# Performance work log

Hardware: AMD Instinct MI355X
Metric: run time of the kernel (lower is better)

## Reference

```python
import jax, jax.numpy as jnp
import numpy as np

S, B, IN, H = 512, 128, 256, 512  # seq_len, batch, input_size, hidden_size


def setup_inputs() -> dict:
    key = jax.random.key(0)
    ks = jax.random.split(key, 17)
    def p(k, shape):
        return jax.random.normal(k, shape, dtype=jnp.float32) * 0.05
    inp = {
        "x": jax.random.normal(ks[0], (S, B, IN), dtype=jnp.float32),
        "h0": jnp.zeros((1, B, H), dtype=jnp.float32),
        "c0": jnp.zeros((1, B, H), dtype=jnp.float32),
    }
    # gates: f=forget, i=input, o=output, g=cell candidate
    for j, n in enumerate(["f", "i", "o", "g"]):
        inp[f"W{n}"] = p(ks[1 + 4 * j], (H, IN))
        inp[f"bW{n}"] = p(ks[2 + 4 * j], (H,))
        inp[f"U{n}"] = p(ks[3 + 4 * j], (H, H))
        inp[f"bU{n}"] = p(ks[4 + 4 * j], (H,))
    return inp


def reference(x, h0, c0, Wf, bWf, Uf, bUf, Wi, bWi, Ui, bUi,
              Wo, bWo, Uo, bUo, Wg, bWg, Ug, bUg):
    # Fuse the 4 input projections and 4 recurrent projections into single GEMMs.
    # Math is identical to applying each Linear separately.
    Wcat = jnp.concatenate([Wf, Wi, Wo, Wg], axis=0)      # [4H, IN]
    bcat = jnp.concatenate([bWf + bUf, bWi + bUi, bWo + bUo, bWg + bUg])  # [4H]
    Ucat = jnp.concatenate([Uf, Ui, Uo, Ug], axis=0)      # [4H, H]
    hd = h0.shape[-1]
    # Precompute input-dependent gate pre-activations for all timesteps.
    xg = jnp.einsum('sbi,gi->sbg', x, Wcat) + bcat        # [S, B, 4H]

    def step(carry, xg_t):
        h, c = carry
        g = xg_t + h @ Ucat.T                             # [B, 4H]
        f = jax.nn.sigmoid(g[..., :hd])
        i = jax.nn.sigmoid(g[..., hd:2 * hd])
        o = jax.nn.sigmoid(g[..., 2 * hd:3 * hd])
        cand = jnp.tanh(g[..., 3 * hd:])
        c = f * c + i * cand
        h = o * jnp.tanh(c)
        return (h, c), h

    (h, c), h_seq = jax.lax.scan(step, (h0[-1], c0[-1]), xg)
    return h_seq, h, c
```

## Files before the change

### kernel.cpp

```cpp
#include <hip/hip_runtime.h>
#include <hip/hip_cooperative_groups.h>

namespace cg = cooperative_groups;


#define SQ   512
#define BB   128
#define IN_  256
#define HH   512
#define RG   8
#define CGN  32
#define RINGHALF (BB * HH)
#define RING_OFF 1024

typedef float    f32x4 __attribute__((ext_vector_type(4)));
typedef short    s16x8 __attribute__((ext_vector_type(8)));
typedef unsigned u32x4 __attribute__((ext_vector_type(4)));

struct P {
  const float *x, *h0, *c0;
  const float *W[4], *bW[4], *U[4], *bU[4];
  float* out;
  unsigned* ring;
  int mode;
};

__device__ __forceinline__ unsigned f2b(float f) {
  unsigned u = __float_as_uint(f);
  return (u + 0x7FFFu + ((u >> 16) & 1u)) >> 16;
}
__device__ __forceinline__ float sigm(float x) { return 1.f / (1.f + __expf(-x)); }
__device__ __forceinline__ float tanh_(float x) {
  float e = __expf(-2.f * fabsf(x));
  float t = (1.f - e) / (1.f + e);
  return copysignf(t, x);
}
__device__ __forceinline__ u32x4 pack8(f32x4 a, f32x4 b) {
  u32x4 d;
  d.x = f2b(a.x) | (f2b(a.y) << 16);
  d.y = f2b(a.z) | (f2b(a.w) << 16);
  d.z = f2b(b.x) | (f2b(b.y) << 16);
  d.w = f2b(b.z) | (f2b(b.w) << 16);
  return d;
}

#define LOAD8_LLC(c0_,c1_,c2_,c3_,c4_,c5_,c6_,c7_,ptr_)                      \
  asm volatile(                                                              \
    "global_load_dwordx4 %0, %8, off sc0 sc1\n\t"                            \
    "global_load_dwordx4 %1, %8, off offset:256 sc0 sc1\n\t"                 \
    "global_load_dwordx4 %2, %8, off offset:512 sc0 sc1\n\t"                 \
    "global_load_dwordx4 %3, %8, off offset:768 sc0 sc1\n\t"                 \
    "global_load_dwordx4 %4, %8, off offset:1024 sc0 sc1\n\t"                \
    "global_load_dwordx4 %5, %8, off offset:1280 sc0 sc1\n\t"                \
    "global_load_dwordx4 %6, %8, off offset:1536 sc0 sc1\n\t"                \
    "global_load_dwordx4 %7, %8, off offset:1792 sc0 sc1\n\t"                \
    "s_waitcnt vmcnt(0)"                                                     \
    : "=&v"(c0_), "=&v"(c1_), "=&v"(c2_), "=&v"(c3_),                        \
      "=&v"(c4_), "=&v"(c5_), "=&v"(c6_), "=&v"(c7_)                         \
    : "v"(ptr_) : "memory")

__global__ void __launch_bounds__(256, 1) lstm_all(P p) {
  __shared__ unsigned short Hs[16][512];
  __shared__ unsigned short Xs[2][16][256];
  __shared__ float gbuf[4][16][17];

  const int tid = threadIdx.x;
  const int bid = blockIdx.x;
  const int r   = bid & 7;
  const int cgi = bid >> 3;
  const int rb  = r * 16;
  const int hcb = cgi * 16;

  const int w   = tid >> 6;
  const int l   = tid & 63;
  const int l16 = l & 15;
  const int lk  = l >> 4;
  const int row16 = tid >> 4;
  const int n16   = tid & 15;

  unsigned* ring = p.ring;

  const int col = hcb + l16;
  s16x8 bfrag[24];
#pragma unroll
  for (int kk = 0; kk < 24; ++kk) {
    int k = kk * 32 + lk * 8;
    const float* src = (kk < 8) ? (p.W[w] + (size_t)col * IN_ + k)
                                : (p.U[w] + (size_t)col * HH + (k - IN_));
    f32x4 a = *(const f32x4*)src;
    f32x4 b = *(const f32x4*)(src + 4);
    s16x8 v;
    v[0]=(short)f2b(a.x); v[1]=(short)f2b(a.y); v[2]=(short)f2b(a.z); v[3]=(short)f2b(a.w);
    v[4]=(short)f2b(b.x); v[5]=(short)f2b(b.y); v[6]=(short)f2b(b.z); v[7]=(short)f2b(b.w);
    bfrag[kk] = v;
  }
  const float bias = p.bW[w][col] + p.bU[w][col];
  float cval = p.c0[(size_t)(rb + row16) * HH + hcb + n16];

  const int wswz = (row16 & 7) << 4;
  const int rswz = (l16 & 7) << 4;
  char* HsB = (char*)&Hs[0][0];
  char* XsB = (char*)&Xs[0][0][0];

  f32x4 xg0, xg1, xg2, xg3;
  {
    const float* xs = p.x + (size_t)(rb + row16) * IN_ + n16 * 16;
    xg0 = *(const f32x4*)(xs);
    xg1 = *(const f32x4*)(xs + 4);
    xg2 = *(const f32x4*)(xs + 8);
    xg3 = *(const f32x4*)(xs + 12);
  }

  for (int t = 0; t < SQ; ++t) {
    {
      char* xrow = XsB + (t & 1) * 8192 + row16 * 512;
      *(u32x4*)(xrow + ((n16 * 32)      ^ wswz)) = pack8(xg0, xg1);
      *(u32x4*)(xrow + ((n16 * 32 + 16) ^ wswz)) = pack8(xg2, xg3);
      if (t + 1 < SQ) {
        const float* xs = p.x + ((size_t)(t + 1) * BB + rb + row16) * IN_ + n16 * 16;
        xg0 = *(const f32x4*)(xs);
        xg1 = *(const f32x4*)(xs + 4);
        xg2 = *(const f32x4*)(xs + 8);
        xg3 = *(const f32x4*)(xs + 12);
      }
    }

    char* hrow = HsB + row16 * 1024;
    if (t == 0) {
      const float* src = p.h0 + (size_t)(rb + row16) * HH + n16 * 4;
#pragma unroll
      for (int cc = 0; cc < 8; ++cc) {
        f32x4 v = *(const f32x4*)(src + cc * 64);
        unsigned lo = f2b(v.x) | (f2b(v.y) << 16);
        unsigned hi = f2b(v.z) | (f2b(v.w) << 16);
        int boff = ((cc * 128 + n16 * 8) ^ wswz);
        *(uint2*)(hrow + boff) = make_uint2(lo, hi);
      }
    } else if (p.mode == 0) {
      const unsigned* hb = ring + (((t - 1) & 1) ? RINGHALF : 0)
                         + (size_t)(rb + row16) * HH + n16 * 4;
      u32x4 c0,c1,c2,c3,c4,c5,c6,c7;
      const unsigned tg = (unsigned)t;
#define TAGOK(v) (((v).x >> 16) == tg && ((v).y >> 16) == tg && \
                  ((v).z >> 16) == tg && ((v).w >> 16) == tg)
      int spin = 0;
      for (;;) {
        LOAD8_LLC(c0,c1,c2,c3,c4,c5,c6,c7,hb);
        if (TAGOK(c0) && TAGOK(c1) && TAGOK(c2) && TAGOK(c3) &&
            TAGOK(c4) && TAGOK(c5) && TAGOK(c6) && TAGOK(c7)) break;
        if (++spin > (1 << 16)) break;
        if (spin > 8) __builtin_amdgcn_s_sleep(1);
      }
#undef TAGOK
      u32x4 cv[8] = {c0,c1,c2,c3,c4,c5,c6,c7};
#pragma unroll
      for (int cc = 0; cc < 8; ++cc) {
        unsigned lo = (cv[cc].x & 0xFFFFu) | (cv[cc].y << 16);
        unsigned hi = (cv[cc].z & 0xFFFFu) | (cv[cc].w << 16);
        int boff = ((cc * 128 + n16 * 8) ^ wswz);
        *(uint2*)(hrow + boff) = make_uint2(lo, hi);
      }
    } else {
      cg::this_grid().sync();
      const float* hp = p.out + ((size_t)(t - 1) * BB + rb + row16) * HH + n16 * 4;
      u32x4 a0,a1,a2,a3,a4,a5,a6,a7;
      LOAD8_LLC(a0,a1,a2,a3,a4,a5,a6,a7,hp);
      u32x4 av[8] = {a0,a1,a2,a3,a4,a5,a6,a7};
#pragma unroll
      for (int cc = 0; cc < 8; ++cc) {
        unsigned lo = f2b(__uint_as_float(av[cc].x)) | (f2b(__uint_as_float(av[cc].y)) << 16);
        unsigned hi = f2b(__uint_as_float(av[cc].z)) | (f2b(__uint_as_float(av[cc].w)) << 16);
        int boff = ((cc * 128 + n16 * 8) ^ wswz);
        *(uint2*)(hrow + boff) = make_uint2(lo, hi);
      }
    }
    __syncthreads();

    f32x4 acc0 = { bias, bias, bias, bias };
    f32x4 acc1 = { 0.f, 0.f, 0.f, 0.f };
    const char* xr = XsB + (t & 1) * 8192 + l16 * 512;
    const char* hr = HsB + l16 * 1024;
#pragma unroll
    for (int kp = 0; kp < 8; kp += 2) {
      s16x8 a0 = *(const s16x8*)(xr + ((kp * 64 + lk * 16)       ^ rswz));
      s16x8 a1 = *(const s16x8*)(xr + (((kp + 1) * 64 + lk * 16) ^ rswz));
      acc0 = __builtin_amdgcn_mfma_f32_16x16x32_bf16(a0, bfrag[kp],     acc0, 0, 0, 0);
      acc1 = __builtin_amdgcn_mfma_f32_16x16x32_bf16(a1, bfrag[kp + 1], acc1, 0, 0, 0);
    }
#pragma unroll
    for (int kp = 0; kp < 16; kp += 2) {
      s16x8 a0 = *(const s16x8*)(hr + ((kp * 64 + lk * 16)       ^ rswz));
      s16x8 a1 = *(const s16x8*)(hr + (((kp + 1) * 64 + lk * 16) ^ rswz));
      acc0 = __builtin_amdgcn_mfma_f32_16x16x32_bf16(a0, bfrag[8 + kp], acc0, 0, 0, 0);
      acc1 = __builtin_amdgcn_mfma_f32_16x16x32_bf16(a1, bfrag[9 + kp], acc1, 0, 0, 0);
    }

#pragma unroll
    for (int rr = 0; rr < 4; ++rr) {
      float v = acc0[rr] + acc1[rr];
      v = (w < 3) ? sigm(v) : tanh_(v);
      gbuf[w][lk * 4 + rr][l16] = v;
    }
    __syncthreads();

    float f = gbuf[0][row16][n16];
    float i = gbuf[1][row16][n16];
    float o = gbuf[2][row16][n16];
    float g = gbuf[3][row16][n16];
    cval = f * cval + i * g;
    float h = o * tanh_(cval);

    size_t oidx = ((size_t)t * BB + rb + row16) * HH + hcb + n16;
    if (p.mode == 0) {
      unsigned tw = ((unsigned)(t + 1) << 16) | f2b(h);
      unsigned* dst = ring + ((t & 1) ? RINGHALF : 0)
                    + (size_t)(rb + row16) * HH + hcb + n16;
      asm volatile("global_store_dword %0, %1, off sc0 sc1"
                   :: "v"(dst), "v"(tw) : "memory");
      __builtin_nontemporal_store(h, p.out + oidx);
    } else {
      asm volatile("global_store_dword %0, %1, off sc0 sc1"
                   :: "v"(p.out + oidx), "v"(h) : "memory");
      asm volatile("s_waitcnt vmcnt(0)" ::: "memory");
    }
    if (t == SQ - 1) {
      size_t base = (size_t)SQ * BB * HH;
      size_t idx2 = (size_t)(rb + row16) * HH + hcb + n16;
      p.out[base + idx2] = h;
      p.out[base + (size_t)BB * HH + idx2] = cval;
    }
  }
}

extern "C" void kernel_launch(void* const* d_in, const int* in_sizes, int n_in,
                              void* d_out, int out_size, void* d_ws, size_t ws_size,
                              hipStream_t stream) {
  P p;
  p.x  = (const float*)d_in[0];
  p.h0 = (const float*)d_in[1];
  p.c0 = (const float*)d_in[2];
  for (int g = 0; g < 4; ++g) {
    p.W[g]  = (const float*)d_in[3 + 4 * g];
    p.bW[g] = (const float*)d_in[4 + 4 * g];
    p.U[g]  = (const float*)d_in[5 + 4 * g];
    p.bU[g] = (const float*)d_in[6 + 4 * g];
  }
  p.out = (float*)d_out;

  const size_t need = (size_t)(RING_OFF + 2 * BB * HH) * sizeof(unsigned);
  const bool ws_ok = (d_ws != nullptr) && (ws_size >= need);
  p.mode = ws_ok ? 0 : 2;
  p.ring = ws_ok ? ((unsigned*)d_ws + RING_OFF) : nullptr;
  if (ws_ok) hipMemsetAsync(d_ws, 0, need, stream);

  void* args[] = { &p };
  hipError_t e = hipLaunchCooperativeKernel((const void*)lstm_all,
                                            dim3(RG * CGN), dim3(256),
                                            args, 0, stream);
  if (e != hipSuccess) {
    hipLaunchKernelGGL(lstm_all, dim3(RG * CGN), dim3(256), 0, stream, p);
  }
}
```

Before: 1.298 ms.

## Replace tagged-word h ring with bf16 ring plus per-wave flag polling

Changes the inter-block handoff of the hidden state. Instead of 32-bit words that carry a step tag beside each bf16 value, blocks now write plain bf16 values to the ring and publish a per-wave step counter after a waitcnt. Readers poll a small flag array and then load their h row with half the bytes in a contiguous layout. This halves ring traffic and makes spin polling cheap. In exchange it adds a waitcnt on every store plus a separate flag-publish round trip. Correctness now depends on memory ordering between the data store and the flag store.

```diff
diff --git a/kernel.cpp b/kernel.cpp
--- a/kernel.cpp
+++ b/kernel.cpp
@@ -10,18 +10,20 @@
 #define HH   512
 #define RG   8
 #define CGN  32
-#define RINGHALF (BB * HH)
-#define RING_OFF 1024
+#define FLAGS_DW   1024
+#define RINGHALF_H (BB * HH)
 
 typedef float    f32x4 __attribute__((ext_vector_type(4)));
 typedef short    s16x8 __attribute__((ext_vector_type(8)));
+typedef unsigned u32x2 __attribute__((ext_vector_type(2)));
 typedef unsigned u32x4 __attribute__((ext_vector_type(4)));
 
 struct P {
   const float *x, *h0, *c0;
   const float *W[4], *bW[4], *U[4], *bU[4];
   float* out;
-  unsigned* ring;
+  unsigned* flags;
+  unsigned short* ring;
   int mode;
 };
 
@@ -43,6 +45,16 @@
   d.w = f2b(b.z) | (f2b(b.w) << 16);
   return d;
 }
+
+#define LOAD4_LLC(c0_,c1_,c2_,c3_,ptr_)                                      \
+  asm volatile(                                                              \
+    "global_load_dwordx4 %0, %4, off sc0 sc1\n\t"                            \
+    "global_load_dwordx4 %1, %4, off offset:16 sc0 sc1\n\t"                  \
+    "global_load_dwordx4 %2, %4, off offset:32 sc0 sc1\n\t"                  \
+    "global_load_dwordx4 %3, %4, off offset:48 sc0 sc1\n\t"                  \
+    "s_waitcnt vmcnt(0)"                                                     \
+    : "=&v"(c0_), "=&v"(c1_), "=&v"(c2_), "=&v"(c3_)                         \
+    : "v"(ptr_) : "memory")
 
 #define LOAD8_LLC(c0_,c1_,c2_,c3_,c4_,c5_,c6_,c7_,ptr_)                      \
   asm volatile(                                                              \
@@ -78,8 +90,6 @@
   const int row16 = tid >> 4;
   const int n16   = tid & 15;
 
-  unsigned* ring = p.ring;
-
   const int col = hcb + l16;
   s16x8 bfrag[24];
 #pragma unroll
@@ -101,6 +111,9 @@
   const int rswz = (l16 & 7) << 4;
   char* HsB = (char*)&Hs[0][0];
   char* XsB = (char*)&Xs[0][0][0];
+
+  const unsigned* fpoll = (p.mode == 0) ? (p.flags + r * 128 + l * 2) : nullptr;
+  unsigned* fpub = (p.mode == 0) ? (p.flags + r * 128 + cgi * 4 + w) : nullptr;
 
   f32x4 xg0, xg1, xg2, xg3;
   {
@@ -127,52 +140,45 @@
 
     char* hrow = HsB + row16 * 1024;
     if (t == 0) {
-      const float* src = p.h0 + (size_t)(rb + row16) * HH + n16 * 4;
-#pragma unroll
-      for (int cc = 0; cc < 8; ++cc) {
-        f32x4 v = *(const f32x4*)(src + cc * 64);
-        unsigned lo = f2b(v.x) | (f2b(v.y) << 16);
-        unsigned hi = f2b(v.z) | (f2b(v.w) << 16);
-        int boff = ((cc * 128 + n16 * 8) ^ wswz);
-        *(uint2*)(hrow + boff) = make_uint2(lo, hi);
+      const float* hs = p.h0 + (size_t)(rb + row16) * HH + n16 * 32;
+#pragma unroll
+      for (int q = 0; q < 4; ++q) {
+        f32x4 a = *(const f32x4*)(hs + q * 8);
+        f32x4 b = *(const f32x4*)(hs + q * 8 + 4);
+        *(u32x4*)(hrow + ((n16 * 64 + q * 16) ^ wswz)) = pack8(a, b);
       }
     } else if (p.mode == 0) {
-      const unsigned* hb = ring + (((t - 1) & 1) ? RINGHALF : 0)
-                         + (size_t)(rb + row16) * HH + n16 * 4;
-      u32x4 c0,c1,c2,c3,c4,c5,c6,c7;
       const unsigned tg = (unsigned)t;
-#define TAGOK(v) (((v).x >> 16) == tg && ((v).y >> 16) == tg && \
-                  ((v).z >> 16) == tg && ((v).w >> 16) == tg)
       int spin = 0;
       for (;;) {
-        LOAD8_LLC(c0,c1,c2,c3,c4,c5,c6,c7,hb);
-        if (TAGOK(c0) && TAGOK(c1) && TAGOK(c2) && TAGOK(c3) &&
-            TAGOK(c4) && TAGOK(c5) && TAGOK(c6) && TAGOK(c7)) break;
-        if (++spin > (1 << 16)) break;
+        u32x2 fv;
+        asm volatile("global_load_dwordx2 %0, %1, off sc0 sc1\n\ts_waitcnt vmcnt(0)"
+                     : "=v"(fv) : "v"(fpoll) : "memory");
+        if (__all((int)(fv.x >= tg && fv.y >= tg))) break;
+        if (++spin > (1 << 13)) break;
         if (spin > 8) __builtin_amdgcn_s_sleep(1);
       }
-#undef TAGOK
-      u32x4 cv[8] = {c0,c1,c2,c3,c4,c5,c6,c7};
-#pragma unroll
-      for (int cc = 0; cc < 8; ++cc) {
-        unsigned lo = (cv[cc].x & 0xFFFFu) | (cv[cc].y << 16);
-        unsigned hi = (cv[cc].z & 0xFFFFu) | (cv[cc].w << 16);
-        int boff = ((cc * 128 + n16 * 8) ^ wswz);
-        *(uint2*)(hrow + boff) = make_uint2(lo, hi);
-      }
+      const unsigned short* hb = p.ring + (size_t)((t - 1) & 1) * RINGHALF_H
+                               + (size_t)(rb + row16) * HH + n16 * 32;
+      u32x4 d0, d1, d2, d3;
+      LOAD4_LLC(d0, d1, d2, d3, hb);
+      *(u32x4*)(hrow + ((n16 * 64)      ^ wswz)) = d0;
+      *(u32x4*)(hrow + ((n16 * 64 + 16) ^ wswz)) = d1;
+      *(u32x4*)(hrow + ((n16 * 64 + 32) ^ wswz)) = d2;
+      *(u32x4*)(hrow + ((n16 * 64 + 48) ^ wswz)) = d3;
     } else {
       cg::this_grid().sync();
-      const float* hp = p.out + ((size_t)(t - 1) * BB + rb + row16) * HH + n16 * 4;
+      const float* hp = p.out + ((size_t)(t - 1) * BB + rb + row16) * HH + n16 * 32;
       u32x4 a0,a1,a2,a3,a4,a5,a6,a7;
       LOAD8_LLC(a0,a1,a2,a3,a4,a5,a6,a7,hp);
-      u32x4 av[8] = {a0,a1,a2,a3,a4,a5,a6,a7};
-#pragma unroll
-      for (int cc = 0; cc < 8; ++cc) {
-        unsigned lo = f2b(__uint_as_float(av[cc].x)) | (f2b(__uint_as_float(av[cc].y)) << 16);
-        unsigned hi = f2b(__uint_as_float(av[cc].z)) | (f2b(__uint_as_float(av[cc].w)) << 16);
-        int boff = ((cc * 128 + n16 * 8) ^ wswz);
-        *(uint2*)(hrow + boff) = make_uint2(lo, hi);
-      }
+      f32x4 av[8];
+      av[0]=__builtin_bit_cast(f32x4,a0); av[1]=__builtin_bit_cast(f32x4,a1);
+      av[2]=__builtin_bit_cast(f32x4,a2); av[3]=__builtin_bit_cast(f32x4,a3);
+      av[4]=__builtin_bit_cast(f32x4,a4); av[5]=__builtin_bit_cast(f32x4,a5);
+      av[6]=__builtin_bit_cast(f32x4,a6); av[7]=__builtin_bit_cast(f32x4,a7);
+#pragma unroll
+      for (int q = 0; q < 4; ++q)
+        *(u32x4*)(hrow + ((n16 * 64 + q * 16) ^ wswz)) = pack8(av[2*q], av[2*q+1]);
     }
     __syncthreads();
 
@@ -212,11 +218,17 @@
 
     size_t oidx = ((size_t)t * BB + rb + row16) * HH + hcb + n16;
     if (p.mode == 0) {
-      unsigned tw = ((unsigned)(t + 1) << 16) | f2b(h);
-      unsigned* dst = ring + ((t & 1) ? RINGHALF : 0)
-                    + (size_t)(rb + row16) * HH + hcb + n16;
-      asm volatile("global_store_dword %0, %1, off sc0 sc1"
-                   :: "v"(dst), "v"(tw) : "memory");
+      unsigned hb16 = f2b(h);
+      unsigned short* dst = p.ring + (size_t)(t & 1) * RINGHALF_H
+                          + (size_t)(rb + row16) * HH + hcb + n16;
+      asm volatile("global_store_short %0, %1, off sc0 sc1"
+                   :: "v"(dst), "v"(hb16) : "memory");
+      asm volatile("s_waitcnt vmcnt(0)" ::: "memory");
+      if ((tid & 63) == 0) {
+        unsigned fv2 = (unsigned)(t + 1);
+        asm volatile("global_store_dword %0, %1, off sc0 sc1"
+                     :: "v"(fpub), "v"(fv2) : "memory");
+      }
       __builtin_nontemporal_store(h, p.out + oidx);
     } else {
       asm volatile("global_store_dword %0, %1, off sc0 sc1"
@@ -247,11 +259,12 @@
   }
   p.out = (float*)d_out;
 
-  const size_t need = (size_t)(RING_OFF + 2 * BB * HH) * sizeof(unsigned);
+  const size_t need = FLAGS_DW * 4 + (size_t)2 * RINGHALF_H * 2;
   const bool ws_ok = (d_ws != nullptr) && (ws_size >= need);
-  p.mode = ws_ok ? 0 : 2;
-  p.ring = ws_ok ? ((unsigned*)d_ws + RING_OFF) : nullptr;
-  if (ws_ok) hipMemsetAsync(d_ws, 0, need, stream);
+  p.mode  = ws_ok ? 0 : 2;
+  p.flags = ws_ok ? (unsigned*)d_ws : nullptr;
+  p.ring  = ws_ok ? (unsigned short*)((unsigned*)d_ws + FLAGS_DW) : nullptr;
+  if (ws_ok) hipMemsetAsync(d_ws, 0, FLAGS_DW * 4, stream);
 
   void* args[] = { &p };
   hipError_t e = hipLaunchCooperativeKernel((const void*)lstm_all,
```

After: 1.671 ms. 1.29x slower.

## Interleave gate columns per wave and double-buffer H to drop a barrier

Applied to the files above, without the earlier changes.

Each wave's 16 MFMA output columns now hold all four gates for 4 hidden units, so the gate combination happens in registers with cross-lane shuffles. This removes the shared-memory gate buffer and the second __syncthreads per timestep. The H tile is double-buffered so the next step's H writes cannot race with reads of the current step, and the X staging is moved after the H wait. In exchange, every lane now computes both sigmoid and tanh, and only a quarter of the lanes (gate 0) perform the global stores.

```diff
diff --git a/kernel.cpp b/kernel.cpp
--- a/kernel.cpp
+++ b/kernel.cpp
@@ -60,9 +60,8 @@
     : "v"(ptr_) : "memory")
 
 __global__ void __launch_bounds__(256, 1) lstm_all(P p) {
-  __shared__ unsigned short Hs[16][512];
+  __shared__ unsigned short Hs[2][16][512];
   __shared__ unsigned short Xs[2][16][256];
-  __shared__ float gbuf[4][16][17];
 
   const int tid = threadIdx.x;
   const int bid = blockIdx.x;
@@ -71,22 +70,26 @@
   const int rb  = r * 16;
   const int hcb = cgi * 16;
 
-  const int w   = tid >> 6;
-  const int l   = tid & 63;
-  const int l16 = l & 15;
-  const int lk  = l >> 4;
+  const int wv   = tid >> 6;
+  const int l    = tid & 63;
+  const int l16  = l & 15;
+  const int lk   = l >> 4;
+  const int gate = l16 >> 2;
+  const int csub = l16 & 3;
   const int row16 = tid >> 4;
   const int n16   = tid & 15;
 
   unsigned* ring = p.ring;
 
-  const int col = hcb + l16;
+  const int col = hcb + wv * 4 + csub;
+  const float* Wg = p.W[gate];
+  const float* Ug = p.U[gate];
   s16x8 bfrag[24];
 #pragma unroll
   for (int kk = 0; kk < 24; ++kk) {
     int k = kk * 32 + lk * 8;
-    const float* src = (kk < 8) ? (p.W[w] + (size_t)col * IN_ + k)
-                                : (p.U[w] + (size_t)col * HH + (k - IN_));
+    const float* src = (kk < 8) ? (Wg + (size_t)col * IN_ + k)
+                                : (Ug + (size_t)col * HH + (k - IN_));
     f32x4 a = *(const f32x4*)src;
     f32x4 b = *(const f32x4*)(src + 4);
     s16x8 v;
@@ -94,13 +97,19 @@
     v[4]=(short)f2b(b.x); v[5]=(short)f2b(b.y); v[6]=(short)f2b(b.z); v[7]=(short)f2b(b.w);
     bfrag[kk] = v;
   }
-  const float bias = p.bW[w][col] + p.bU[w][col];
-  float cval = p.c0[(size_t)(rb + row16) * HH + hcb + n16];
+  const float bias = p.bW[gate][col] + p.bU[gate][col];
+
+  f32x4 cv;
+#pragma unroll
+  for (int rr = 0; rr < 4; ++rr)
+    cv[rr] = p.c0[(size_t)(rb + lk * 4 + rr) * HH + col];
 
   const int wswz = (row16 & 7) << 4;
   const int rswz = (l16 & 7) << 4;
-  char* HsB = (char*)&Hs[0][0];
+  char* HsB = (char*)&Hs[0][0][0];
   char* XsB = (char*)&Xs[0][0][0];
+  const bool b2 = (gate & 1) != 0;
+  const bool b3 = (gate & 2) != 0;
 
   f32x4 xg0, xg1, xg2, xg3;
   {
@@ -112,20 +121,9 @@
   }
 
   for (int t = 0; t < SQ; ++t) {
-    {
-      char* xrow = XsB + (t & 1) * 8192 + row16 * 512;
-      *(u32x4*)(xrow + ((n16 * 32)      ^ wswz)) = pack8(xg0, xg1);
-      *(u32x4*)(xrow + ((n16 * 32 + 16) ^ wswz)) = pack8(xg2, xg3);
-      if (t + 1 < SQ) {
-        const float* xs = p.x + ((size_t)(t + 1) * BB + rb + row16) * IN_ + n16 * 16;
-        xg0 = *(const f32x4*)(xs);
-        xg1 = *(const f32x4*)(xs + 4);
-        xg2 = *(const f32x4*)(xs + 8);
-        xg3 = *(const f32x4*)(xs + 12);
-      }
-    }
-
-    char* hrow = HsB + row16 * 1024;
+    const int half = t & 1;
+
+    char* hrow = HsB + half * 16384 + row16 * 1024;
     if (t == 0) {
       const float* src = p.h0 + (size_t)(rb + row16) * HH + n16 * 4;
 #pragma unroll
@@ -152,11 +150,11 @@
         if (spin > 8) __builtin_amdgcn_s_sleep(1);
       }
 #undef TAGOK
-      u32x4 cv[8] = {c0,c1,c2,c3,c4,c5,c6,c7};
+      u32x4 cvv[8] = {c0,c1,c2,c3,c4,c5,c6,c7};
 #pragma unroll
       for (int cc = 0; cc < 8; ++cc) {
-        unsigned lo = (cv[cc].x & 0xFFFFu) | (cv[cc].y << 16);
-        unsigned hi = (cv[cc].z & 0xFFFFu) | (cv[cc].w << 16);
+        unsigned lo = (cvv[cc].x & 0xFFFFu) | (cvv[cc].y << 16);
+        unsigned hi = (cvv[cc].z & 0xFFFFu) | (cvv[cc].w << 16);
         int boff = ((cc * 128 + n16 * 8) ^ wswz);
         *(uint2*)(hrow + boff) = make_uint2(lo, hi);
       }
@@ -174,12 +172,25 @@
         *(uint2*)(hrow + boff) = make_uint2(lo, hi);
       }
     }
+
+    {
+      char* xrow = XsB + half * 8192 + row16 * 512;
+      *(u32x4*)(xrow + ((n16 * 32)      ^ wswz)) = pack8(xg0, xg1);
+      *(u32x4*)(xrow + ((n16 * 32 + 16) ^ wswz)) = pack8(xg2, xg3);
+      if (t + 1 < SQ) {
+        const float* xs = p.x + ((size_t)(t + 1) * BB + rb + row16) * IN_ + n16 * 16;
+        xg0 = *(const f32x4*)(xs);
+        xg1 = *(const f32x4*)(xs + 4);
+        xg2 = *(const f32x4*)(xs + 8);
+        xg3 = *(const f32x4*)(xs + 12);
+      }
+    }
     __syncthreads();
 
     f32x4 acc0 = { bias, bias, bias, bias };
     f32x4 acc1 = { 0.f, 0.f, 0.f, 0.f };
-    const char* xr = XsB + (t & 1) * 8192 + l16 * 512;
-    const char* hr = HsB + l16 * 1024;
+    const char* xr = XsB + half * 8192  + l16 * 512;
+    const char* hr = HsB + half * 16384 + l16 * 1024;
 #pragma unroll
     for (int kp = 0; kp < 8; kp += 2) {
       s16x8 a0 = *(const s16x8*)(xr + ((kp * 64 + lk * 16)       ^ rswz));
@@ -195,39 +206,57 @@
       acc1 = __builtin_amdgcn_mfma_f32_16x16x32_bf16(a1, bfrag[9 + kp], acc1, 0, 0, 0);
     }
 
+    float hv[4];
 #pragma unroll
     for (int rr = 0; rr < 4; ++rr) {
-      float v = acc0[rr] + acc1[rr];
-      v = (w < 3) ? sigm(v) : tanh_(v);
-      gbuf[w][lk * 4 + rr][l16] = v;
-    }
-    __syncthreads();
-
-    float f = gbuf[0][row16][n16];
-    float i = gbuf[1][row16][n16];
-    float o = gbuf[2][row16][n16];
-    float g = gbuf[3][row16][n16];
-    cval = f * cval + i * g;
-    float h = o * tanh_(cval);
-
-    size_t oidx = ((size_t)t * BB + rb + row16) * HH + hcb + n16;
+      float v  = acc0[rr] + acc1[rr];
+      float sg = sigm(v);
+      float th = tanh_(v);
+      float va = (b2 && b3) ? th : sg;
+      float x1 = __shfl_xor(va, 4);
+      float x2 = __shfl_xor(va, 8);
+      float x3 = __shfl_xor(va, 12);
+      float fg = b3 ? (b2 ? x3 : x2) : (b2 ? x1 : va);
+      float ig = b3 ? (b2 ? x2 : x3) : (b2 ? va : x1);
+      float og = b3 ? (b2 ? x1 : va) : (b2 ? x3 : x2);
+      float gg = b3 ? (b2 ? va : x1) : (b2 ? x2 : x3);
+      cv[rr] = fg * cv[rr] + ig * gg;
+      hv[rr] = og * tanh_(cv[rr]);
+    }
+
     if (p.mode == 0) {
-      unsigned tw = ((unsigned)(t + 1) << 16) | f2b(h);
-      unsigned* dst = ring + ((t & 1) ? RINGHALF : 0)
-                    + (size_t)(rb + row16) * HH + hcb + n16;
-      asm volatile("global_store_dword %0, %1, off sc0 sc1"
-                   :: "v"(dst), "v"(tw) : "memory");
-      __builtin_nontemporal_store(h, p.out + oidx);
+      if (gate == 0) {
+#pragma unroll
+        for (int rr = 0; rr < 4; ++rr) {
+          int row = rb + lk * 4 + rr;
+          unsigned tw = ((unsigned)(t + 1) << 16) | f2b(hv[rr]);
+          unsigned* dst = ring + (half ? RINGHALF : 0) + (size_t)row * HH + col;
+          asm volatile("global_store_dword %0, %1, off sc0 sc1"
+                       :: "v"(dst), "v"(tw) : "memory");
+          __builtin_nontemporal_store(hv[rr],
+              p.out + ((size_t)t * BB + row) * HH + col);
+        }
+      }
     } else {
-      asm volatile("global_store_dword %0, %1, off sc0 sc1"
-                   :: "v"(p.out + oidx), "v"(h) : "memory");
+      if (gate == 0) {
+#pragma unroll
+        for (int rr = 0; rr < 4; ++rr) {
+          int row = rb + lk * 4 + rr;
+          asm volatile("global_store_dword %0, %1, off sc0 sc1"
+                       :: "v"(p.out + ((size_t)t * BB + row) * HH + col),
+                          "v"(hv[rr]) : "memory");
+        }
+      }
       asm volatile("s_waitcnt vmcnt(0)" ::: "memory");
     }
-    if (t == SQ - 1) {
+    if (t == SQ - 1 && gate == 0) {
       size_t base = (size_t)SQ * BB * HH;
-      size_t idx2 = (size_t)(rb + row16) * HH + hcb + n16;
-      p.out[base + idx2] = h;
-      p.out[base + (size_t)BB * HH + idx2] = cval;
+#pragma unroll
+      for (int rr = 0; rr < 4; ++rr) {
+        size_t idx2 = (size_t)(rb + lk * 4 + rr) * HH + col;
+        p.out[base + idx2] = hv[rr];
+        p.out[base + (size_t)BB * HH + idx2] = cv[rr];
+      }
     }
   }
 }
```

Measured after the change: 3.148 ms. +142.6%, slower.

## Halve grid to 128 blocks of 512 threads, each owning 32 hidden columns

Applied to the files above, without the earlier changes.

Block count drops from 256 to 128 and each block doubles to 512 threads (8 waves: 4 gates x 2 column tiles), so each block computes 32 hidden columns instead of 16. The h-staging loads and ring polling are reshaped so each thread reads 16 contiguous values. This halves the number of blocks that redundantly load the shared x/h rows and poll the ring each step, cutting inter-block synchronization traffic. In exchange, each CU does twice the MFMA work per step and the per-step critical path per block may grow.

```diff
diff --git a/kernel.cpp b/kernel.cpp
--- a/kernel.cpp
+++ b/kernel.cpp
@@ -9,7 +9,7 @@
 #define IN_  256
 #define HH   512
 #define RG   8
-#define CGN  32
+#define CGN  16
 #define RINGHALF (BB * HH)
 #define RING_OFF 1024
 
@@ -44,49 +44,48 @@
   return d;
 }
 
-#define LOAD8_LLC(c0_,c1_,c2_,c3_,c4_,c5_,c6_,c7_,ptr_)                      \
+#define LOAD4_LLC(c0_,c1_,c2_,c3_,ptr_)                                      \
   asm volatile(                                                              \
-    "global_load_dwordx4 %0, %8, off sc0 sc1\n\t"                            \
-    "global_load_dwordx4 %1, %8, off offset:256 sc0 sc1\n\t"                 \
-    "global_load_dwordx4 %2, %8, off offset:512 sc0 sc1\n\t"                 \
-    "global_load_dwordx4 %3, %8, off offset:768 sc0 sc1\n\t"                 \
-    "global_load_dwordx4 %4, %8, off offset:1024 sc0 sc1\n\t"                \
-    "global_load_dwordx4 %5, %8, off offset:1280 sc0 sc1\n\t"                \
-    "global_load_dwordx4 %6, %8, off offset:1536 sc0 sc1\n\t"                \
-    "global_load_dwordx4 %7, %8, off offset:1792 sc0 sc1\n\t"                \
+    "global_load_dwordx4 %0, %4, off sc0 sc1\n\t"                            \
+    "global_load_dwordx4 %1, %4, off offset:16 sc0 sc1\n\t"                  \
+    "global_load_dwordx4 %2, %4, off offset:32 sc0 sc1\n\t"                  \
+    "global_load_dwordx4 %3, %4, off offset:48 sc0 sc1\n\t"                  \
     "s_waitcnt vmcnt(0)"                                                     \
-    : "=&v"(c0_), "=&v"(c1_), "=&v"(c2_), "=&v"(c3_),                        \
-      "=&v"(c4_), "=&v"(c5_), "=&v"(c6_), "=&v"(c7_)                         \
+    : "=&v"(c0_), "=&v"(c1_), "=&v"(c2_), "=&v"(c3_)                         \
     : "v"(ptr_) : "memory")
 
-__global__ void __launch_bounds__(256, 1) lstm_all(P p) {
+__global__ void __launch_bounds__(512, 1) lstm_all(P p) {
   __shared__ unsigned short Hs[16][512];
   __shared__ unsigned short Xs[2][16][256];
-  __shared__ float gbuf[4][16][17];
+  __shared__ float gbuf[4][16][33];
 
   const int tid = threadIdx.x;
   const int bid = blockIdx.x;
   const int r   = bid & 7;
   const int cgi = bid >> 3;
   const int rb  = r * 16;
-  const int hcb = cgi * 16;
-
-  const int w   = tid >> 6;
-  const int l   = tid & 63;
-  const int l16 = l & 15;
-  const int lk  = l >> 4;
-  const int row16 = tid >> 4;
-  const int n16   = tid & 15;
+  const int hcb = cgi * 32;
+
+  const int w8   = tid >> 6;
+  const int gate = w8 >> 1;
+  const int ct   = w8 & 1;
+  const int l    = tid & 63;
+  const int l16  = l & 15;
+  const int lk   = l >> 4;
+  const int srow = tid >> 5;
+  const int sn   = tid & 31;
 
   unsigned* ring = p.ring;
 
-  const int col = hcb + l16;
+  const int colb = hcb + ct * 16 + l16;
+  const float* Wg = p.W[gate];
+  const float* Ug = p.U[gate];
   s16x8 bfrag[24];
 #pragma unroll
   for (int kk = 0; kk < 24; ++kk) {
     int k = kk * 32 + lk * 8;
-    const float* src = (kk < 8) ? (p.W[w] + (size_t)col * IN_ + k)
-                                : (p.U[w] + (size_t)col * HH + (k - IN_));
+    const float* src = (kk < 8) ? (Wg + (size_t)colb * IN_ + k)
+                                : (Ug + (size_t)colb * HH + (k - IN_));
     f32x4 a = *(const f32x4*)src;
     f32x4 b = *(const f32x4*)(src + 4);
     s16x8 v;
@@ -94,85 +93,78 @@
     v[4]=(short)f2b(b.x); v[5]=(short)f2b(b.y); v[6]=(short)f2b(b.z); v[7]=(short)f2b(b.w);
     bfrag[kk] = v;
   }
-  const float bias = p.bW[w][col] + p.bU[w][col];
-  float cval = p.c0[(size_t)(rb + row16) * HH + hcb + n16];
-
-  const int wswz = (row16 & 7) << 4;
+  const float bias = p.bW[gate][colb] + p.bU[gate][colb];
+  float cval = p.c0[(size_t)(rb + srow) * HH + hcb + sn];
+
+  const int wswz = (srow & 7) << 4;
   const int rswz = (l16 & 7) << 4;
   char* HsB = (char*)&Hs[0][0];
   char* XsB = (char*)&Xs[0][0][0];
 
-  f32x4 xg0, xg1, xg2, xg3;
+  f32x4 xg0, xg1;
   {
-    const float* xs = p.x + (size_t)(rb + row16) * IN_ + n16 * 16;
+    const float* xs = p.x + (size_t)(rb + srow) * IN_ + sn * 8;
     xg0 = *(const f32x4*)(xs);
     xg1 = *(const f32x4*)(xs + 4);
-    xg2 = *(const f32x4*)(xs + 8);
-    xg3 = *(const f32x4*)(xs + 12);
   }
 
   for (int t = 0; t < SQ; ++t) {
     {
-      char* xrow = XsB + (t & 1) * 8192 + row16 * 512;
-      *(u32x4*)(xrow + ((n16 * 32)      ^ wswz)) = pack8(xg0, xg1);
-      *(u32x4*)(xrow + ((n16 * 32 + 16) ^ wswz)) = pack8(xg2, xg3);
+      char* xrow = XsB + (t & 1) * 8192 + srow * 512;
+      *(u32x4*)(xrow + ((sn * 16) ^ wswz)) = pack8(xg0, xg1);
       if (t + 1 < SQ) {
-        const float* xs = p.x + ((size_t)(t + 1) * BB + rb + row16) * IN_ + n16 * 16;
+        const float* xs = p.x + ((size_t)(t + 1) * BB + rb + srow) * IN_ + sn * 8;
         xg0 = *(const f32x4*)(xs);
         xg1 = *(const f32x4*)(xs + 4);
-        xg2 = *(const f32x4*)(xs + 8);
-        xg3 = *(const f32x4*)(xs + 12);
       }
     }
 
-    char* hrow = HsB + row16 * 1024;
+    char* hrow = HsB + srow * 1024;
     if (t == 0) {
-      const float* src = p.h0 + (size_t)(rb + row16) * HH + n16 * 4;
-#pragma unroll
-      for (int cc = 0; cc < 8; ++cc) {
-        f32x4 v = *(const f32x4*)(src + cc * 64);
-        unsigned lo = f2b(v.x) | (f2b(v.y) << 16);
-        unsigned hi = f2b(v.z) | (f2b(v.w) << 16);
-        int boff = ((cc * 128 + n16 * 8) ^ wswz);
-        *(uint2*)(hrow + boff) = make_uint2(lo, hi);
-      }
+      const float* hs = p.h0 + (size_t)(rb + srow) * HH + sn * 16;
+      f32x4 a0 = *(const f32x4*)(hs);
+      f32x4 b0 = *(const f32x4*)(hs + 4);
+      f32x4 a1 = *(const f32x4*)(hs + 8);
+      f32x4 b1 = *(const f32x4*)(hs + 12);
+      *(u32x4*)(hrow + ((sn * 32)      ^ wswz)) = pack8(a0, b0);
+      *(u32x4*)(hrow + ((sn * 32 + 16) ^ wswz)) = pack8(a1, b1);
     } else if (p.mode == 0) {
       const unsigned* hb = ring + (((t - 1) & 1) ? RINGHALF : 0)
-                         + (size_t)(rb + row16) * HH + n16 * 4;
-      u32x4 c0,c1,c2,c3,c4,c5,c6,c7;
+                         + (size_t)(rb + srow) * HH + sn * 16;
+      u32x4 c0, c1, c2, c3;
       const unsigned tg = (unsigned)t;
 #define TAGOK(v) (((v).x >> 16) == tg && ((v).y >> 16) == tg && \
                   ((v).z >> 16) == tg && ((v).w >> 16) == tg)
       int spin = 0;
       for (;;) {
-        LOAD8_LLC(c0,c1,c2,c3,c4,c5,c6,c7,hb);
-        if (TAGOK(c0) && TAGOK(c1) && TAGOK(c2) && TAGOK(c3) &&
-            TAGOK(c4) && TAGOK(c5) && TAGOK(c6) && TAGOK(c7)) break;
+        LOAD4_LLC(c0, c1, c2, c3, hb);
+        if (TAGOK(c0) && TAGOK(c1) && TAGOK(c2) && TAGOK(c3)) break;
         if (++spin > (1 << 16)) break;
         if (spin > 8) __builtin_amdgcn_s_sleep(1);
       }
 #undef TAGOK
-      u32x4 cv[8] = {c0,c1,c2,c3,c4,c5,c6,c7};
-#pragma unroll
-      for (int cc = 0; cc < 8; ++cc) {
-        unsigned lo = (cv[cc].x & 0xFFFFu) | (cv[cc].y << 16);
-        unsigned hi = (cv[cc].z & 0xFFFFu) | (cv[cc].w << 16);
-        int boff = ((cc * 128 + n16 * 8) ^ wswz);
-        *(uint2*)(hrow + boff) = make_uint2(lo, hi);
-      }
+      u32x4 w0, w1;
+      w0.x = (c0.x & 0xFFFFu) | (c0.y << 16);
+      w0.y = (c0.z & 0xFFFFu) | (c0.w << 16);
+      w0.z = (c1.x & 0xFFFFu) | (c1.y << 16);
+      w0.w = (c1.z & 0xFFFFu) | (c1.w << 16);
+      w1.x = (c2.x & 0xFFFFu) | (c2.y << 16);
+      w1.y = (c2.z & 0xFFFFu) | (c2.w << 16);
+      w1.z = (c3.x & 0xFFFFu) | (c3.y << 16);
+      w1.w = (c3.z & 0xFFFFu) | (c3.w << 16);
+      *(u32x4*)(hrow + ((sn * 32)      ^ wswz)) = w0;
+      *(u32x4*)(hrow + ((sn * 32 + 16) ^ wswz)) = w1;
     } else {
       cg::this_grid().sync();
-      const float* hp = p.out + ((size_t)(t - 1) * BB + rb + row16) * HH + n16 * 4;
-      u32x4 a0,a1,a2,a3,a4,a5,a6,a7;
-      LOAD8_LLC(a0,a1,a2,a3,a4,a5,a6,a7,hp);
-      u32x4 av[8] = {a0,a1,a2,a3,a4,a5,a6,a7};
-#pragma unroll
-      for (int cc = 0; cc < 8; ++cc) {
-        unsigned lo = f2b(__uint_as_float(av[cc].x)) | (f2b(__uint_as_float(av[cc].y)) << 16);
-        unsigned hi = f2b(__uint_as_float(av[cc].z)) | (f2b(__uint_as_float(av[cc].w)) << 16);
-        int boff = ((cc * 128 + n16 * 8) ^ wswz);
-        *(uint2*)(hrow + boff) = make_uint2(lo, hi);
-      }
+      const float* hp = p.out + ((size_t)(t - 1) * BB + rb + srow) * HH + sn * 16;
+      u32x4 a0, a1, a2, a3;
+      LOAD4_LLC(a0, a1, a2, a3, hp);
+      f32x4 f0 = __builtin_bit_cast(f32x4, a0);
+      f32x4 f1 = __builtin_bit_cast(f32x4, a1);
+      f32x4 f2 = __builtin_bit_cast(f32x4, a2);
+      f32x4 f3 = __builtin_bit_cast(f32x4, a3);
+      *(u32x4*)(hrow + ((sn * 32)      ^ wswz)) = pack8(f0, f1);
+      *(u32x4*)(hrow + ((sn * 32 + 16) ^ wswz)) = pack8(f2, f3);
     }
     __syncthreads();
 
@@ -198,23 +190,23 @@
 #pragma unroll
     for (int rr = 0; rr < 4; ++rr) {
       float v = acc0[rr] + acc1[rr];
-      v = (w < 3) ? sigm(v) : tanh_(v);
-      gbuf[w][lk * 4 + rr][l16] = v;
+      v = (gate < 3) ? sigm(v) : tanh_(v);
+      gbuf[gate][lk * 4 + rr][ct * 16 + l16] = v;
     }
     __syncthreads();
 
-    float f = gbuf[0][row16][n16];
-    float i = gbuf[1][row16][n16];
-    float o = gbuf[2][row16][n16];
-    float g = gbuf[3][row16][n16];
+    float f = gbuf[0][srow][sn];
+    float i = gbuf[1][srow][sn];
+    float o = gbuf[2][srow][sn];
+    float g = gbuf[3][srow][sn];
     cval = f * cval + i * g;
     float h = o * tanh_(cval);
 
-    size_t oidx = ((size_t)t * BB + rb + row16) * HH + hcb + n16;
+    size_t oidx = ((size_t)t * BB + rb + srow) * HH + hcb + sn;
     if (p.mode == 0) {
       unsigned tw = ((unsigned)(t + 1) << 16) | f2b(h);
       unsigned* dst = ring + ((t & 1) ? RINGHALF : 0)
-                    + (size_t)(rb + row16) * HH + hcb + n16;
+                    + (size_t)(rb + srow) * HH + hcb + sn;
       asm volatile("global_store_dword %0, %1, off sc0 sc1"
                    :: "v"(dst), "v"(tw) : "memory");
       __builtin_nontemporal_store(h, p.out + oidx);
@@ -225,7 +217,7 @@
     }
     if (t == SQ - 1) {
       size_t base = (size_t)SQ * BB * HH;
-      size_t idx2 = (size_t)(rb + row16) * HH + hcb + n16;
+      size_t idx2 = (size_t)(rb + srow) * HH + hcb + sn;
       p.out[base + idx2] = h;
       p.out[base + (size_t)BB * HH + idx2] = cval;
     }
@@ -255,9 +247,9 @@
 
   void* args[] = { &p };
   hipError_t e = hipLaunchCooperativeKernel((const void*)lstm_all,
-                                            dim3(RG * CGN), dim3(256),
+                                            dim3(RG * CGN), dim3(512),
                                             args, 0, stream);
   if (e != hipSuccess) {
-    hipLaunchKernelGGL(lstm_all, dim3(RG * CGN), dim3(256), 0, stream, p);
-  }
-}
+    hipLaunchKernelGGL(lstm_all, dim3(RG * CGN), dim3(512), 0, stream, p);
+  }
+}
```

After: 1.479 ms. 13.9% more time.
